# Kernel tuning notes

Hardware: AMD Instinct MI355X
Metric: run time of the kernel (lower is better)

## Reference

```python
import jax, jax.numpy as jnp
import numpy as np

B, CIN, H, W = 16, 256, 56, 56
D, HEADS, KS, PAD, STRIDE, M = 256, 8, 3, 1, 1, 4
K = KS * KS
N = D // HEADS
# relative_indices: sum of window coords, flattened row-major, values in [0, 2*KS-2]
REL = (np.arange(KS)[:, None] + np.arange(KS)[None, :]).reshape(-1)


def setup_inputs() -> dict:
    key = jax.random.key(0)
    ks = jax.random.split(key, 7)
    return {
        "x": jax.random.normal(ks[0], (B, CIN, H, W), jnp.float32),
        "q": jax.random.normal(ks[1], (B, D, 1), jnp.float32),
        "Wk": jax.random.normal(ks[2], (D, CIN), jnp.float32) * 0.05,
        "Wv": jax.random.normal(ks[3], (D, CIN), jnp.float32) * 0.05,
        "pos_emb": jax.random.normal(ks[4], (1, 2 * KS - 1), jnp.float32),
        "Wlin": jax.random.normal(ks[5], (1, M), jnp.float32),
        "Wproj": jax.random.normal(ks[6], (D, D), jnp.float32) * 0.05,
    }


def _unfold(t):
    # torch nn.Unfold: (B,C,H,W) -> (B, C*K, L); patches feature dim ordered (C, kh, kw)
    p = jax.lax.conv_general_dilated_patches(
        t, (KS, KS), (STRIDE, STRIDE), [(PAD, PAD), (PAD, PAD)])
    b, _, ho, wo = p.shape
    return p.reshape(b, -1, ho * wo), ho, wo


def reference(x, q, Wk, Wv, pos_emb, Wlin, Wproj):
    b = x.shape[0]
    k = jnp.einsum('oc,bchw->bohw', Wk, x)  # 1x1 conv, no bias
    v = jnp.einsum('oc,bchw->bohw', Wv, x)
    ku, ho, wo = _unfold(k)
    vu, _, _ = _unfold(v)
    L = ho * wo
    ku = ku.reshape(b, HEADS, N, K, L)  # (b, h, n, k, l)
    vu = vu.reshape(b, HEADS, N, K, L)
    qh = q.reshape(b, HEADS, N)  # learned per-batch query, d=1 squeezed
    attn = jnp.einsum('bhn,bhnkl->bhlk', qh, ku)  # (b,h,l,K)
    attn = attn + pos_emb[0, REL]  # relative position bias, shape (K,)
    attn = jax.nn.softmax(attn, axis=-1)
    # repeat d(=1) -> m identical rows then Linear(m,1,no bias): equals scale by sum(Wlin)
    attn = attn * jnp.sum(Wlin)
    out = jnp.einsum('bhlk,bhnkl->bhnl', attn, vu)  # (b,h,n,l)
    out = out.reshape(b, D, ho, wo)  # fold with kernel 1 == reshape
    return jnp.einsum('oc,bchw->bohw', Wproj, out)  # 1x1 proj conv
```

## Files before the change

kernel.cpp:

```cpp
#include <hip/hip_runtime.h>

#define B_     16
#define D_     256
#define HEADS_ 8
#define N_     32
#define H_     56
#define W_     56
#define L_     3136
#define BL_    (B_ * L_)

typedef short short8 __attribute__((ext_vector_type(8)));
typedef float f32x4  __attribute__((ext_vector_type(4)));

__device__ __forceinline__ unsigned short f2bf(float f) {
    union { float f; unsigned u; } c; c.f = f;
    unsigned u = c.u;
    u += 0x7fffu + ((u >> 16) & 1u);
    return (unsigned short)(u >> 16);
}

#define GL2L(g, l) __builtin_amdgcn_global_load_lds( \
    (const __attribute__((address_space(1))) void*)(g), \
    (__attribute__((address_space(3))) void*)(l), 16, 0, 0)

__global__ __launch_bounds__(256) void convert_w_kernel(
    const float* __restrict__ Wv, const float* __restrict__ Wproj,
    const float* __restrict__ Wk, const float* __restrict__ q,
    unsigned short* __restrict__ Wvb, unsigned short* __restrict__ Wpb,
    float* __restrict__ qt)
{
    if (blockIdx.y < 2) {
        const float* src   = (blockIdx.y == 0) ? Wv  : Wproj;
        unsigned short* dst = (blockIdx.y == 0) ? Wvb : Wpb;
        const int i = (blockIdx.x * 256 + threadIdx.x) * 4;
        float4 v = *(const float4*)(src + i);
        uint2 o;
        o.x = (unsigned)f2bf(v.x) | ((unsigned)f2bf(v.y) << 16);
        o.y = (unsigned)f2bf(v.z) | ((unsigned)f2bf(v.w) << 16);
        *(uint2*)(dst + i) = o;
    } else {
        const int b  = blockIdx.x >> 2;
        const int h0 = (blockIdx.x & 3) * 2;
        const int c  = threadIdx.x;
#pragma unroll
        for (int hh = 0; hh < 2; ++hh) {
            const int h = h0 + hh;
            const float* qb = q  + b * D_ + h * N_;
            const float* wr = Wk + (size_t)(h * N_) * D_ + c;
            float acc = 0.f;
#pragma unroll 8
            for (int n = 0; n < N_; ++n)
                acc = fmaf(qb[n], wr[(size_t)n * D_], acc);
            qt[((size_t)b * HEADS_ + h) * D_ + c] = acc;
        }
    }
}

__global__ __launch_bounds__(256) void transpose_x_kernel(
    const float* __restrict__ x, unsigned short* __restrict__ Xt)
{
    __shared__ float tile[64][65];
    const int bb = blockIdx.z;
    const int c0 = blockIdx.y * 64;
    const int l0 = blockIdx.x * 64;
    const int t  = threadIdx.x;
    const int g4 = (t & 15) * 4;
    const int rr = t >> 4;

    const float* xb = x + ((size_t)bb * D_ + c0) * L_ + l0;
#pragma unroll
    for (int i = 0; i < 4; ++i) {
        const int c = rr + i * 16;
        float4 v = *(const float4*)(xb + (size_t)c * L_ + g4);
        *(float4*)&tile[c][g4] = v;
    }
    __syncthreads();
    unsigned short* Xb = Xt + ((size_t)bb * L_ + l0) * D_ + c0;
#pragma unroll
    for (int i = 0; i < 4; ++i) {
        const int l = rr + i * 16;
        uint2 o;
        o.x = (unsigned)f2bf(tile[g4 + 0][l]) | ((unsigned)f2bf(tile[g4 + 1][l]) << 16);
        o.y = (unsigned)f2bf(tile[g4 + 2][l]) | ((unsigned)f2bf(tile[g4 + 3][l]) << 16);
        *(uint2*)(Xb + (size_t)l * D_ + g4) = o;
    }
}

__global__ __launch_bounds__(256) void s_kernel(
    const float* __restrict__ x, const float* __restrict__ qt,
    float* __restrict__ S)
{
    __shared__ float qs[HEADS_ * D_];
    __shared__ float red[4][HEADS_][64];

    const int bb = blockIdx.y;
    const int l0 = blockIdx.x * 64;
    const int t  = threadIdx.x;
    const int sl = t & 63;
    const int cq = t >> 6;

    {
        const float4* s4 = (const float4*)(qt + (size_t)bb * HEADS_ * D_);
        ((float4*)qs)[t]       = s4[t];
        ((float4*)qs)[t + 256] = s4[t + 256];
    }
    __syncthreads();

    float sacc[8];
#pragma unroll
    for (int h = 0; h < 8; ++h) sacc[h] = 0.f;

    const float* xb = x + (size_t)bb * D_ * L_ + l0 + sl;
#pragma unroll 4
    for (int c = cq * 64; c < cq * 64 + 64; ++c) {
        const float xv = xb[(size_t)c * L_];
#pragma unroll
        for (int h = 0; h < 8; ++h)
            sacc[h] = fmaf(qs[h * D_ + c], xv, sacc[h]);
    }

#pragma unroll
    for (int h = 0; h < 8; ++h) red[cq][h][sl] = sacc[h];
    __syncthreads();

    const int h0 = t >> 6;
#pragma unroll
    for (int r = 0; r < 2; ++r) {
        const int h = h0 + r * 4;
        const float s = red[0][h][sl] + red[1][h][sl] + red[2][h][sl] + red[3][h][sl];
        S[((size_t)bb * HEADS_ + h) * L_ + l0 + sl] = s;
    }
}

__global__ __launch_bounds__(256) void gemm_v_mfma(
    const unsigned short* __restrict__ Xt, const unsigned short* __restrict__ Wvb,
    unsigned short* __restrict__ Vo)
{
    __shared__ unsigned short As[2][128 * 32];
    __shared__ unsigned short Bs[2][128 * 32];

    const int t = threadIdx.x;
    const int w = t >> 6, lane = t & 63, col = lane & 15, quad = lane >> 4;
    const int wr = w >> 1, wc = w & 1;
    const int n0 = blockIdx.x * 128;
    const int d0 = blockIdx.y * 128;
    const int srow = t >> 2;
    const int skc  = (t & 3) * 8;

    const unsigned short* Ag = Wvb + (size_t)(d0 + srow) * D_ + skc;
    const unsigned short* Bg = Xt + (size_t)(n0 + srow) * D_ + skc;

    f32x4 acc[4][4];
#pragma unroll
    for (int m = 0; m < 4; ++m)
#pragma unroll
        for (int n = 0; n < 4; ++n) acc[m][n] = (f32x4){0.f, 0.f, 0.f, 0.f};

    {
        char* An = (char*)&As[0][0] + w * 1024;
        char* Bn = (char*)&Bs[0][0] + w * 1024;
        GL2L(Ag, An);            GL2L(Ag + 64 * D_, An + 4096);
        GL2L(Bg, Bn);            GL2L(Bg + 64 * D_, Bn + 4096);
    }
    __syncthreads();

#pragma unroll
    for (int kt = 0; kt < 8; ++kt) {
        const int cur = kt & 1;
        if (kt < 7) {
            const int c1 = (kt + 1) * 32;
            char* An = (char*)&As[cur ^ 1][0] + w * 1024;
            char* Bn = (char*)&Bs[cur ^ 1][0] + w * 1024;
            GL2L(Ag + c1, An);           GL2L(Ag + 64 * D_ + c1, An + 4096);
            GL2L(Bg + c1, Bn);           GL2L(Bg + 64 * D_ + c1, Bn + 4096);
        }
        const unsigned short* Ab = &As[cur][0];
        const unsigned short* Bb = &Bs[cur][0];
        short8 af[4], bf[4];
#pragma unroll
        for (int m = 0; m < 4; ++m)
            af[m] = *(const short8*)(Ab + (wr * 64 + m * 16 + col) * 32 + quad * 8);
#pragma unroll
        for (int n = 0; n < 4; ++n)
            bf[n] = *(const short8*)(Bb + (wc * 64 + n * 16 + col) * 32 + quad * 8);
#pragma unroll
        for (int m = 0; m < 4; ++m)
#pragma unroll
            for (int n = 0; n < 4; ++n)
                acc[m][n] = __builtin_amdgcn_mfma_f32_16x16x32_bf16(af[m], bf[n], acc[m][n], 0, 0, 0);
        __syncthreads();
    }

#pragma unroll
    for (int n = 0; n < 4; ++n) {
        const unsigned flat = n0 + wc * 64 + n * 16 + col;
        const unsigned bq = flat / L_;
        const unsigned lq = flat - bq * L_;
#pragma unroll
        for (int m = 0; m < 4; ++m) {
            const int d  = d0 + wr * 64 + m * 16 + quad * 4;
            const int h  = d >> 5;
            const int dn = d & 31;
            unsigned short ob[4];
#pragma unroll
            for (int r = 0; r < 4; ++r) ob[r] = f2bf(acc[m][n][r]);
            *(uint2*)(Vo + ((size_t)(bq * HEADS_ + h) * L_ + lq) * N_ + dn) =
                *(const uint2*)ob;
        }
    }
}

__global__ __launch_bounds__(256) void attend_kernel(
    const float* __restrict__ S, const unsigned short* __restrict__ Vo,
    const float* __restrict__ pos_emb, const float* __restrict__ Wlin,
    unsigned short* __restrict__ Om)
{
    __shared__ __align__(16) unsigned short Vs[10][60][8];
    __shared__ float Ss[10][58];

    const int band = blockIdx.x;
    const int half = blockIdx.y;
    const int bh   = blockIdx.z;
    const int y0   = band * 8;
    const int t    = threadIdx.x;

    const float* Sb = S + (size_t)bh * L_;
    for (int wi = t; wi < 580; wi += 256) {
        const int row = wi / 58, c = wi - row * 58;
        const int gr = y0 - 1 + row, gc = c - 1;
        float v = 0.f;
        if (gr >= 0 && gr < H_ && gc >= 0 && gc < W_)
            v = Sb[gr * W_ + gc];
        Ss[row][c] = v;
    }

    const unsigned short* Vbase = Vo + (size_t)bh * L_ * N_ + half * 8;
    for (int wi = t; wi < 580; wi += 256) {
        const int row = wi / 58, c = wi - row * 58;
        const int gr = y0 - 1 + row, gc = c - 1;
        uint4 v = make_uint4(0u, 0u, 0u, 0u);
        if (gr >= 0 && gr < H_ && gc >= 0 && gc < W_)
            v = *(const uint4*)(Vbase + (size_t)(gr * W_ + gc) * N_);
        *(uint4*)&Vs[row][c][0] = v;
    }
    __syncthreads();

    const float scale = Wlin[0] + Wlin[1] + Wlin[2] + Wlin[3];
    const float pe0 = pos_emb[0], pe1 = pos_emb[1], pe2 = pos_emb[2];
    const float pe3 = pos_emb[3], pe4 = pos_emb[4];
    const float bias[9] = {pe0, pe1, pe2, pe1, pe2, pe3, pe2, pe3, pe4};

    for (int p = t; p < 448; p += 256) {
        const int yl = p / 56, xx = p - yl * 56;
        const int lr = yl + 1, lc = xx + 1;

        float lg[9], m = -1e30f;
#pragma unroll
        for (int dy = 0; dy < 3; ++dy)
#pragma unroll
            for (int dx = 0; dx < 3; ++dx) {
                const int k = dy * 3 + dx;
                lg[k] = Ss[lr - 1 + dy][lc - 1 + dx] + bias[k];
                m = fmaxf(m, lg[k]);
            }
        float ssum = 0.f;
#pragma unroll
        for (int k = 0; k < 9; ++k) { lg[k] = __expf(lg[k] - m); ssum += lg[k]; }
        const float inv = scale / ssum;

        float om[8] = {0.f, 0.f, 0.f, 0.f, 0.f, 0.f, 0.f, 0.f};
#pragma unroll
        for (int dy = 0; dy < 3; ++dy)
#pragma unroll
            for (int dx = 0; dx < 3; ++dx) {
                const float wk = lg[dy * 3 + dx] * inv;
                const uint4 v = *(const uint4*)&Vs[lr - 1 + dy][lc - 1 + dx][0];
                const unsigned* u = (const unsigned*)&v;
#pragma unroll
                for (int i = 0; i < 4; ++i) {
                    union { unsigned uu; float f; } lo, hi;
                    lo.uu = u[i] << 16;
                    hi.uu = u[i] & 0xffff0000u;
                    om[2 * i]     = fmaf(wk, lo.f, om[2 * i]);
                    om[2 * i + 1] = fmaf(wk, hi.f, om[2 * i + 1]);
                }
            }

        unsigned short ob[8];
#pragma unroll
        for (int i = 0; i < 8; ++i) ob[i] = f2bf(om[i]);
        const int l = (y0 + yl) * W_ + xx;
        *(uint4*)(Om + ((size_t)bh * L_ + l) * N_ + half * 8) = *(const uint4*)ob;
    }
}

__global__ __launch_bounds__(256) void gemm_proj_mfma(
    const unsigned short* __restrict__ Om, const unsigned short* __restrict__ Wpb,
    float* __restrict__ Out)
{
    __shared__ unsigned short As[2][128 * 32];
    __shared__ unsigned short Bs[2][128 * 32];

    const int t = threadIdx.x;
    const int w = t >> 6, lane = t & 63, col = lane & 15, quad = lane >> 4;
    const int wr = w >> 1, wc = w & 1;
    const int n0 = blockIdx.x * 128;
    const int d0 = blockIdx.y * 128;
    const int srow = t >> 2;
    const int skc  = (t & 3) * 8;

    const unsigned short* Ag = Wpb + (size_t)(d0 + srow) * D_ + skc;
    const int f0 = n0 + srow;
    const unsigned b0q = (unsigned)f0 / L_, l0q = (unsigned)f0 - b0q * L_;
    const int f1 = f0 + 64;
    const unsigned b1q = (unsigned)f1 / L_, l1q = (unsigned)f1 - b1q * L_;
    const unsigned short* Bg0 = Om + ((size_t)(b0q * HEADS_) * L_ + l0q) * N_ + skc;
    const unsigned short* Bg1 = Om + ((size_t)(b1q * HEADS_) * L_ + l1q) * N_ + skc;
    const size_t kstride = (size_t)L_ * N_;

    f32x4 acc[4][4];
#pragma unroll
    for (int m = 0; m < 4; ++m)
#pragma unroll
        for (int n = 0; n < 4; ++n) acc[m][n] = (f32x4){0.f, 0.f, 0.f, 0.f};

    {
        char* An = (char*)&As[0][0] + w * 1024;
        char* Bn = (char*)&Bs[0][0] + w * 1024;
        GL2L(Ag, An);            GL2L(Ag + 64 * D_, An + 4096);
        GL2L(Bg0, Bn);           GL2L(Bg1, Bn + 4096);
    }
    __syncthreads();

#pragma unroll
    for (int kt = 0; kt < 8; ++kt) {
        const int cur = kt & 1;
        if (kt < 7) {
            const int c1 = (kt + 1) * 32;
            char* An = (char*)&As[cur ^ 1][0] + w * 1024;
            char* Bn = (char*)&Bs[cur ^ 1][0] + w * 1024;
            GL2L(Ag + c1, An);                     GL2L(Ag + 64 * D_ + c1, An + 4096);
            GL2L(Bg0 + (kt + 1) * kstride, Bn);    GL2L(Bg1 + (kt + 1) * kstride, Bn + 4096);
        }
        const unsigned short* Ab = &As[cur][0];
        const unsigned short* Bb = &Bs[cur][0];
        short8 af[4], bf[4];
#pragma unroll
        for (int m = 0; m < 4; ++m)
            af[m] = *(const short8*)(Ab + (wr * 64 + m * 16 + col) * 32 + quad * 8);
#pragma unroll
        for (int n = 0; n < 4; ++n)
            bf[n] = *(const short8*)(Bb + (wc * 64 + n * 16 + col) * 32 + quad * 8);
#pragma unroll
        for (int m = 0; m < 4; ++m)
#pragma unroll
            for (int n = 0; n < 4; ++n)
                acc[m][n] = __builtin_amdgcn_mfma_f32_16x16x32_bf16(af[m], bf[n], acc[m][n], 0, 0, 0);
        __syncthreads();
    }

#pragma unroll
    for (int n = 0; n < 4; ++n) {
        const unsigned flat = n0 + wc * 64 + n * 16 + col;
        const unsigned bq = flat / L_;
        const unsigned lq = flat - bq * L_;
        float* oout = Out + (size_t)bq * D_ * L_ + lq;
#pragma unroll
        for (int m = 0; m < 4; ++m) {
            const int dbase = d0 + wr * 64 + m * 16 + quad * 4;
#pragma unroll
            for (int r = 0; r < 4; ++r)
                oout[(size_t)(dbase + r) * L_] = acc[m][n][r];
        }
    }
}

extern "C" void kernel_launch(void* const* d_in, const int* in_sizes, int n_in,
                              void* d_out, int out_size, void* d_ws, size_t ws_size,
                              hipStream_t stream)
{
    const float* x       = (const float*)d_in[0];
    const float* q       = (const float*)d_in[1];
    const float* Wk      = (const float*)d_in[2];
    const float* Wv      = (const float*)d_in[3];
    const float* pos_emb = (const float*)d_in[4];
    const float* Wlin    = (const float*)d_in[5];
    const float* Wproj   = (const float*)d_in[6];
    float* out = (float*)d_out;

    const size_t planeE = (size_t)B_ * D_ * L_;
    unsigned short* Xt  = (unsigned short*)d_ws;
    unsigned short* Vo  = Xt + planeE;
    unsigned short* Om  = Vo + planeE;
    unsigned short* Wvb = Om + planeE;
    unsigned short* Wpb = Wvb + D_ * D_;
    float*          S   = (float*)(Wpb + D_ * D_);
    float*          qt  = S + (size_t)B_ * HEADS_ * L_;

    convert_w_kernel<<<dim3(64, 3), 256, 0, stream>>>(Wv, Wproj, Wk, q, Wvb, Wpb, qt);
    transpose_x_kernel<<<dim3(L_ / 64, D_ / 64, B_), 256, 0, stream>>>(x, Xt);
    s_kernel<<<dim3(L_ / 64, B_), 256, 0, stream>>>(x, qt, S);
    gemm_v_mfma<<<dim3(BL_ / 128, 2), 256, 0, stream>>>(Xt, Wvb, Vo);
    attend_kernel<<<dim3(7, 4, B_ * HEADS_), 256, 0, stream>>>(S, Vo, pos_emb, Wlin, Om);
    gemm_proj_mfma<<<dim3(BL_ / 128, 2), 256, 0, stream>>>(Om, Wpb, out);
}
```

Baseline: 191.1 us.

## Vectorize s_kernel over four pixels and process all 32 channels per attend block

s_kernel now has each thread compute four adjacent pixels using float4 loads of x. This cuts the grid by a factor of four and reuses each shared-memory q read across four FMAs. attend_kernel drops the 4-way channel split: one block stages the full 32-channel V halo tile in an XOR-swizzled LDS layout, and each thread computes the softmax once and applies it to all 32 channels. The aim is to stop recomputing the softmax and reloading S across the four channel quarters. The cost is more registers per thread (32 accumulators), a larger LDS footprint and fewer blocks, which may reduce occupancy.

```diff
diff --git a/kernel.cpp b/kernel.cpp
--- a/kernel.cpp
+++ b/kernel.cpp
@@ -90,11 +90,11 @@
     const float* __restrict__ x, const float* __restrict__ qt,
     float* __restrict__ S)
 {
-    __shared__ float qs[HEADS_ * D_];
-    __shared__ float red[4][HEADS_][64];
+    __shared__ float  qs[HEADS_ * D_];
+    __shared__ float4 red[4][HEADS_ * 64];
 
     const int bb = blockIdx.y;
-    const int l0 = blockIdx.x * 64;
+    const int l0 = blockIdx.x * 256;
     const int t  = threadIdx.x;
     const int sl = t & 63;
     const int cq = t >> 6;
@@ -106,29 +106,46 @@
     }
     __syncthreads();
 
-    float sacc[8];
-#pragma unroll
-    for (int h = 0; h < 8; ++h) sacc[h] = 0.f;
-
-    const float* xb = x + (size_t)bb * D_ * L_ + l0 + sl;
+    float4 sacc[8];
+#pragma unroll
+    for (int h = 0; h < 8; ++h) sacc[h] = (float4){0.f, 0.f, 0.f, 0.f};
+
+    const int l = l0 + sl * 4;
+    if (l < L_) {
+        const float* xb = x + (size_t)bb * D_ * L_ + l;
 #pragma unroll 4
-    for (int c = cq * 64; c < cq * 64 + 64; ++c) {
-        const float xv = xb[(size_t)c * L_];
-#pragma unroll
-        for (int h = 0; h < 8; ++h)
-            sacc[h] = fmaf(qs[h * D_ + c], xv, sacc[h]);
-    }
-
-#pragma unroll
-    for (int h = 0; h < 8; ++h) red[cq][h][sl] = sacc[h];
-    __syncthreads();
-
-    const int h0 = t >> 6;
-#pragma unroll
-    for (int r = 0; r < 2; ++r) {
-        const int h = h0 + r * 4;
-        const float s = red[0][h][sl] + red[1][h][sl] + red[2][h][sl] + red[3][h][sl];
-        S[((size_t)bb * HEADS_ + h) * L_ + l0 + sl] = s;
+        for (int c = cq * 64; c < cq * 64 + 64; ++c) {
+            const float4 xv = *(const float4*)(xb + (size_t)c * L_);
+#pragma unroll
+            for (int h = 0; h < 8; ++h) {
+                const float qv = qs[h * D_ + c];
+                sacc[h].x = fmaf(qv, xv.x, sacc[h].x);
+                sacc[h].y = fmaf(qv, xv.y, sacc[h].y);
+                sacc[h].z = fmaf(qv, xv.z, sacc[h].z);
+                sacc[h].w = fmaf(qv, xv.w, sacc[h].w);
+            }
+        }
+    }
+
+#pragma unroll
+    for (int h = 0; h < 8; ++h) red[cq][h * 64 + sl] = sacc[h];
+    __syncthreads();
+
+    for (int j = t; j < 512; j += 256) {
+        const int h = j >> 6, s = j & 63;
+        const int lw = l0 + s * 4;
+        if (lw < L_) {
+            const float4 a = red[0][h * 64 + s];
+            const float4 b = red[1][h * 64 + s];
+            const float4 c = red[2][h * 64 + s];
+            const float4 d = red[3][h * 64 + s];
+            float4 o;
+            o.x = a.x + b.x + c.x + d.x;
+            o.y = a.y + b.y + c.y + d.y;
+            o.z = a.z + b.z + c.z + d.z;
+            o.w = a.w + b.w + c.w + d.w;
+            *(float4*)(S + ((size_t)bb * HEADS_ + h) * L_ + lw) = o;
+        }
     }
 }
 
@@ -215,12 +232,11 @@
     const float* __restrict__ pos_emb, const float* __restrict__ Wlin,
     unsigned short* __restrict__ Om)
 {
-    __shared__ __align__(16) unsigned short Vs[10][60][8];
+    __shared__ __align__(16) unsigned short Vs[600 * 32];
     __shared__ float Ss[10][58];
 
     const int band = blockIdx.x;
-    const int half = blockIdx.y;
-    const int bh   = blockIdx.z;
+    const int bh   = blockIdx.y;
     const int y0   = band * 8;
     const int t    = threadIdx.x;
 
@@ -234,14 +250,16 @@
         Ss[row][c] = v;
     }
 
-    const unsigned short* Vbase = Vo + (size_t)bh * L_ * N_ + half * 8;
-    for (int wi = t; wi < 580; wi += 256) {
-        const int row = wi / 58, c = wi - row * 58;
-        const int gr = y0 - 1 + row, gc = c - 1;
+    const unsigned short* Vbase = Vo + (size_t)bh * L_ * N_;
+    for (int wi = t; wi < 2400; wi += 256) {
+        const int p = wi >> 2, i = wi & 3;
+        const int row = p / 60, cc = p - row * 60;
+        const int gr = y0 - 1 + row, gc = cc - 1;
         uint4 v = make_uint4(0u, 0u, 0u, 0u);
         if (gr >= 0 && gr < H_ && gc >= 0 && gc < W_)
-            v = *(const uint4*)(Vbase + (size_t)(gr * W_ + gc) * N_);
-        *(uint4*)&Vs[row][c][0] = v;
+            v = *(const uint4*)(Vbase + (size_t)(gr * W_ + gc) * N_ + i * 8);
+        const int sfc = wi ^ (p & 7);
+        *(uint4*)(Vs + sfc * 8) = v;
     }
     __syncthreads();
 
@@ -250,8 +268,8 @@
     const float pe3 = pos_emb[3], pe4 = pos_emb[4];
     const float bias[9] = {pe0, pe1, pe2, pe1, pe2, pe3, pe2, pe3, pe4};
 
-    for (int p = t; p < 448; p += 256) {
-        const int yl = p / 56, xx = p - yl * 56;
+    for (int idx = t; idx < 448; idx += 256) {
+        const int yl = idx / 56, xx = idx - yl * 56;
         const int lr = yl + 1, lc = xx + 1;
 
         float lg[9], m = -1e30f;
@@ -268,29 +286,42 @@
         for (int k = 0; k < 9; ++k) { lg[k] = __expf(lg[k] - m); ssum += lg[k]; }
         const float inv = scale / ssum;
 
-        float om[8] = {0.f, 0.f, 0.f, 0.f, 0.f, 0.f, 0.f, 0.f};
+        float om[32];
+#pragma unroll
+        for (int i = 0; i < 32; ++i) om[i] = 0.f;
+
 #pragma unroll
         for (int dy = 0; dy < 3; ++dy)
 #pragma unroll
             for (int dx = 0; dx < 3; ++dx) {
                 const float wk = lg[dy * 3 + dx] * inv;
-                const uint4 v = *(const uint4*)&Vs[lr - 1 + dy][lc - 1 + dx][0];
-                const unsigned* u = (const unsigned*)&v;
+                const int pos  = (lr - 1 + dy) * 60 + (lc - 1 + dx);
+                const int base = pos * 4;
+                const int msk  = pos & 7;
 #pragma unroll
                 for (int i = 0; i < 4; ++i) {
-                    union { unsigned uu; float f; } lo, hi;
-                    lo.uu = u[i] << 16;
-                    hi.uu = u[i] & 0xffff0000u;
-                    om[2 * i]     = fmaf(wk, lo.f, om[2 * i]);
-                    om[2 * i + 1] = fmaf(wk, hi.f, om[2 * i + 1]);
+                    const int sfc = (base + i) ^ msk;
+                    const uint4 v = *(const uint4*)(Vs + sfc * 8);
+                    const unsigned* u = (const unsigned*)&v;
+#pragma unroll
+                    for (int j = 0; j < 4; ++j) {
+                        union { unsigned uu; float f; } lo, hi;
+                        lo.uu = u[j] << 16;
+                        hi.uu = u[j] & 0xffff0000u;
+                        om[i * 8 + 2 * j]     = fmaf(wk, lo.f, om[i * 8 + 2 * j]);
+                        om[i * 8 + 2 * j + 1] = fmaf(wk, hi.f, om[i * 8 + 2 * j + 1]);
+                    }
                 }
             }
 
-        unsigned short ob[8];
-#pragma unroll
-        for (int i = 0; i < 8; ++i) ob[i] = f2bf(om[i]);
+        unsigned short ob[32];
+#pragma unroll
+        for (int i = 0; i < 32; ++i) ob[i] = f2bf(om[i]);
         const int l = (y0 + yl) * W_ + xx;
-        *(uint4*)(Om + ((size_t)bh * L_ + l) * N_ + half * 8) = *(const uint4*)ob;
+        uint4* dst = (uint4*)(Om + ((size_t)bh * L_ + l) * N_);
+        const uint4* sb = (const uint4*)ob;
+#pragma unroll
+        for (int i = 0; i < 4; ++i) dst[i] = sb[i];
     }
 }
 
@@ -399,8 +430,8 @@
 
     convert_w_kernel<<<dim3(64, 3), 256, 0, stream>>>(Wv, Wproj, Wk, q, Wvb, Wpb, qt);
     transpose_x_kernel<<<dim3(L_ / 64, D_ / 64, B_), 256, 0, stream>>>(x, Xt);
-    s_kernel<<<dim3(L_ / 64, B_), 256, 0, stream>>>(x, qt, S);
+    s_kernel<<<dim3((L_ + 255) / 256, B_), 256, 0, stream>>>(x, qt, S);
     gemm_v_mfma<<<dim3(BL_ / 128, 2), 256, 0, stream>>>(Xt, Wvb, Vo);
-    attend_kernel<<<dim3(7, 4, B_ * HEADS_), 256, 0, stream>>>(S, Vo, pos_emb, Wlin, Om);
+    attend_kernel<<<dim3(7, B_ * HEADS_), 256, 0, stream>>>(S, Vo, pos_emb, Wlin, Om);
     gemm_proj_mfma<<<dim3(BL_ / 128, 2), 256, 0, stream>>>(Om, Wpb, out);
 }
```

After: 177.2 us. 7.2% less time.
